# Performance work log

Hardware: AMD Instinct MI355X
Metric: run time of the kernel (lower is better)

## Reference

```python
import jax, jax.numpy as jnp
from jax import lax
import numpy as np

GROUPS = 32  # EMA 'factor'
EPS = 1e-5   # torch GroupNorm default eps


def setup_inputs() -> dict:
    key = jax.random.key(0)
    ks = jax.random.split(key, 3)
    B, C, H, W = 8, 256, 128, 128
    cg = C // GROUPS  # channels per group = 8
    x = jax.random.normal(ks[0], (B, C, H, W), dtype=jnp.float32)
    w1 = jax.random.normal(ks[1], (cg, cg), dtype=jnp.float32) * 0.1    # conv1x1 weight (O,I)
    b1 = jnp.zeros((cg,), dtype=jnp.float32)
    w3 = jax.random.normal(ks[2], (cg, cg, 3, 3), dtype=jnp.float32) * 0.1  # conv3x3 weight (O,I,kh,kw)
    b3 = jnp.zeros((cg,), dtype=jnp.float32)
    gn_w = jnp.ones((cg,), dtype=jnp.float32)
    gn_b = jnp.zeros((cg,), dtype=jnp.float32)
    return {"x": x, "w1": w1, "b1": b1, "w3": w3, "b3": b3, "gn_w": gn_w, "gn_b": gn_b}


def reference(x, w1, b1, w3, b3, gn_w, gn_b):
    b, c, h, w = x.shape
    g = GROUPS
    cg = c // g
    gx = x.reshape(b * g, cg, h, w)                       # [bg, cg, h, w]
    # directional pooling (AdaptiveAvgPool over one axis)
    x_h = gx.mean(axis=3, keepdims=True)                  # [bg, cg, h, 1]
    x_w = gx.mean(axis=2, keepdims=True).transpose(0, 1, 3, 2)  # [bg, cg, w, 1]
    hw = jnp.concatenate([x_h, x_w], axis=2)              # [bg, cg, h+w, 1]
    hw = jnp.einsum('oi,bilk->bolk', w1, hw) + b1[None, :, None, None]
    xh = hw[:, :, :h]                                      # [bg, cg, h, 1]
    xw = hw[:, :, h:].transpose(0, 1, 3, 2)                # [bg, cg, 1, w]
    gated = gx * jax.nn.sigmoid(xh) * jax.nn.sigmoid(xw)
    # GroupNorm(cg groups over cg channels) == per-channel norm over (h, w)
    mu = gated.mean(axis=(2, 3), keepdims=True)
    var = gated.var(axis=(2, 3), keepdims=True)
    x1 = (gated - mu) / jnp.sqrt(var + EPS) * gn_w[None, :, None, None] + gn_b[None, :, None, None]
    # 3x3 conv branch
    x2 = lax.conv_general_dilated(gx, w3, (1, 1), 'SAME',
                                  dimension_numbers=('NCHW', 'OIHW', 'NCHW'))
    x2 = x2 + b3[None, :, None, None]
    # cross-branch channel-attention matmuls
    x11 = jax.nn.softmax(x1.mean(axis=(2, 3)), axis=-1)[:, None, :]  # [bg, 1, cg]
    x21 = jax.nn.softmax(x2.mean(axis=(2, 3)), axis=-1)[:, None, :]  # [bg, 1, cg]
    x12 = x2.reshape(b * g, cg, h * w)
    x22 = x1.reshape(b * g, cg, h * w)
    weights = (jnp.matmul(x11, x12) + jnp.matmul(x21, x22)).reshape(b * g, 1, h, w)
    return (gx * jax.nn.sigmoid(weights)).reshape(b, c, h, w)
```

## Files before the change

kernel.cpp:

```cpp
#include <hip/hip_runtime.h>
#include <cstdint>

#define EPS 1e-5f

__global__ __launch_bounds__(256) void k1_sums(const float* __restrict__ x,
                                               float* __restrict__ rowsum,
                                               float* __restrict__ colsum) {
    int p = blockIdx.x;
    int t = threadIdx.x;
    const float4* xp = (const float4*)(x + (size_t)p * 16384);
    float4 csum = {0.f, 0.f, 0.f, 0.f};
    for (int i = 0; i < 16; ++i) {
        float4 v = xp[i * 256 + t];
        csum.x += v.x; csum.y += v.y; csum.z += v.z; csum.w += v.w;
        float rs = v.x + v.y + v.z + v.w;
        for (int m = 16; m; m >>= 1) rs += __shfl_xor(rs, m);
        if ((t & 31) == 0) rowsum[p * 128 + i * 8 + (t >> 5)] = rs;
    }
    __shared__ float4 red[256];
    red[t] = csum;
    __syncthreads();
    if (t < 32) {
        float4 s = red[t];
        for (int j = 1; j < 8; ++j) {
            float4 v = red[j * 32 + t];
            s.x += v.x; s.y += v.y; s.z += v.z; s.w += v.w;
        }
        ((float4*)colsum)[p * 32 + t] = s;
    }
}

__global__ __launch_bounds__(1024) void k2_mid(
    const float* __restrict__ x,
    const float* __restrict__ rowsum, const float* __restrict__ colsum,
    const float* __restrict__ w1, const float* __restrict__ b1,
    const float* __restrict__ w3, const float* __restrict__ b3,
    const float* __restrict__ gn_w, const float* __restrict__ gn_b,
    float* __restrict__ sh, float* __restrict__ sw,
    float* __restrict__ wt, float* __restrict__ alpha, float* __restrict__ beta)
{
    __shared__ float rs[1024], cs[1024], shl[1024], swl[1024];
    __shared__ float w1l[64], b1l[8], corn[32], S[8], Tm[72], m2[8], x11[8], x21l[8];
    __shared__ float ps[64], qs[64], bs[8];
    __shared__ float btl;
    const int bg = blockIdx.x;
    const int t  = threadIdx.x;
    const int sg = t >> 8, ts = t & 255;
    const size_t pbase = (size_t)(bg * 8) * 16384;

    rs[t] = rowsum[bg * 1024 + t];
    cs[t] = colsum[bg * 1024 + t];
    if (t < 64) w1l[t] = w1[t];
    if (t >= 64 && t < 72) b1l[t - 64] = b1[t - 64];
    if (t >= 128 && t < 136) {
        int i = t - 128;
        const float* xpp = x + pbase + (size_t)i * 16384;
        corn[i * 4 + 0] = xpp[0];
        corn[i * 4 + 1] = xpp[127];
        corn[i * 4 + 2] = xpp[127 * 128];
        corn[i * 4 + 3] = xpp[127 * 128 + 127];
    }
    if (t == 200) {
        float mx = gn_b[0];
        for (int i = 1; i < 8; ++i) mx = fmaxf(mx, gn_b[i]);
        float e[8], s = 0.f;
        for (int i = 0; i < 8; ++i) { e[i] = __expf(gn_b[i] - mx); s += e[i]; }
        for (int i = 0; i < 8; ++i) x11[i] = e[i] / s;
    }
    __syncthreads();

    if (t == 300) {
        float a = 0.f;
        for (int o = 0; o < 8; ++o) a += x11[o] * b3[o];
        btl = a;
    }
    {
        int o = t >> 7, y = t & 127;
        const float inv128 = 1.f / 128.f;
        float ar = b1l[o], ac = ar;
        for (int i = 0; i < 8; ++i) {
            float w = w1l[o * 8 + i];
            ar += w * rs[i * 128 + y] * inv128;
            ac += w * cs[i * 128 + y] * inv128;
        }
        float sv = 1.f / (1.f + __expf(-ar));
        float wv = 1.f / (1.f + __expf(-ac));
        shl[o * 128 + y] = sv;  sh[(bg * 8 + o) * 128 + y] = sv;
        swl[o * 128 + y] = wv;  sw[(bg * 8 + o) * 128 + y] = wv;
    }
    if (t < 8) {
        float s = 0.f;
        for (int y = 0; y < 128; ++y) s += rs[t * 128 + y];
        S[t] = s;
    }
    __syncthreads();

    if (t < 72) {
        int i = t / 9, ky = (t % 9) / 3, kx = t % 3;
        float v = S[i];
        if (ky == 0) v -= rs[i * 128 + 127]; else if (ky == 2) v -= rs[i * 128 + 0];
        if (kx == 0) v -= cs[i * 128 + 127]; else if (kx == 2) v -= cs[i * 128 + 0];
        if (ky == 0 && kx == 0) v += corn[i * 4 + 3];
        if (ky == 0 && kx == 2) v += corn[i * 4 + 2];
        if (ky == 2 && kx == 0) v += corn[i * 4 + 1];
        if (ky == 2 && kx == 2) v += corn[i * 4 + 0];
        Tm[t] = v;
    }
    __syncthreads();

    if (t < 8) {
        float acc = 0.f;
        for (int j = 0; j < 72; ++j) acc += w3[t * 72 + j] * Tm[j];
        m2[t] = b3[t] + acc * (1.f / 16384.f);
    }
    if (bg == 0 && t >= 128 && t < 200) {
        int j = t - 128;
        float a = 0.f;
        for (int o = 0; o < 8; ++o) a += x11[o] * w3[o * 72 + j];
        wt[j] = a;
    }
    __syncthreads();

    if (t == 0) {
        float mx = m2[0];
        for (int i = 1; i < 8; ++i) mx = fmaxf(mx, m2[i]);
        float e[8], s = 0.f;
        for (int i = 0; i < 8; ++i) { e[i] = __expf(m2[i] - mx); s += e[i]; }
        for (int i = 0; i < 8; ++i) x21l[i] = e[i] / s;
    }
    __syncthreads();

    for (int half = 0; half < 2; ++half) {
        int pi = half * 4 + sg;
        const float4* xp = (const float4*)(x + pbase + (size_t)pi * 16384);
        float4 sw4 = ((const float4*)(swl + pi * 128))[ts & 31];
        float s = 0.f, q = 0.f;
        for (int i = 0; i < 16; ++i) {
            float4 v = xp[i * 256 + ts];
            float shv = shl[pi * 128 + i * 8 + (ts >> 5)];
            float g0 = v.x * shv * sw4.x;
            float g1 = v.y * shv * sw4.y;
            float g2 = v.z * shv * sw4.z;
            float g3 = v.w * shv * sw4.w;
            s += g0 + g1 + g2 + g3;
            q += g0 * g0 + g1 * g1 + g2 * g2 + g3 * g3;
        }
        for (int m = 16; m; m >>= 1) { s += __shfl_xor(s, m); q += __shfl_xor(q, m); }
        if ((ts & 31) == 0) {
            ps[pi * 8 + (ts >> 5)] = s;
            qs[pi * 8 + (ts >> 5)] = q;
        }
    }
    __syncthreads();
    if (t < 8) {
        float s = 0.f, q = 0.f;
        for (int j = 0; j < 8; ++j) { s += ps[t * 8 + j]; q += qs[t * 8 + j]; }
        float mu  = s * (1.f / 16384.f);
        float ex2 = q * (1.f / 16384.f);
        float var = ex2 - mu * mu;
        float inv = rsqrtf(var + EPS);
        float x21v = x21l[t];
        alpha[bg * 8 + t] = x21v * inv * gn_w[t];
        bs[t] = x21v * (gn_b[t] - mu * inv * gn_w[t]);
    }
    __syncthreads();
    if (t == 0) {
        float s = btl;
        for (int i = 0; i < 8; ++i) s += bs[i];
        beta[bg] = s;
    }
}

__global__ __launch_bounds__(512, 4) void k3_out(
    const float* __restrict__ x, const float* __restrict__ sh,
    const float* __restrict__ sw, const float* __restrict__ alpha,
    const float* __restrict__ beta, const float* __restrict__ wt,
    float* __restrict__ out)
{
    __shared__ float tl[8 * 18 * 128];
    __shared__ float wtl[72], al[8], shl[128];
    __shared__ float betal;
    const int blk = blockIdx.x, bg = blk >> 3, r0 = (blk & 7) * 16;
    const int t = threadIdx.x, lane = t & 31, w = t >> 5;
    const size_t pbase = (size_t)(bg * 8) * 16384;

#pragma unroll
    for (int it = 0; it < 9; ++it) {
        int idx = it * 512 + t;
        int ch  = idx / 576;
        int rem = idx - ch * 576;
        int row = rem >> 5;
        int slot = rem & 31;
        int g = r0 - 1 + row;
        float4 v = {0.f, 0.f, 0.f, 0.f};
        if ((unsigned)g < 128u)
            v = *(const float4*)(x + pbase + (size_t)ch * 16384 + g * 128 + slot * 4);
        *(float4*)(tl + ch * 2304 + row * 128 + slot * 4) = v;
    }
    if (t < 72) wtl[t] = wt[t];
    if (t >= 128 && t < 136) al[t - 128] = alpha[bg * 8 + (t - 128)];
    if (t == 136) betal = beta[bg];
    if (t >= 256 && t < 384) {
        int u = t - 256;
        shl[u] = sh[(size_t)(bg * 8 + (u >> 4)) * 128 + r0 + (u & 15)];
    }
    __syncthreads();

    const int y  = r0 + w;
    const int x0 = lane * 4;
    float4 acc = {betal, betal, betal, betal};
    float4 gv[8];

#pragma unroll
    for (int ch = 0; ch < 8; ++ch) {
        const float* base = tl + ch * 2304 + w * 128 + x0;
#pragma unroll
        for (int r = 0; r < 3; ++r) {
            float4 va = *(const float4*)(base + r * 128);
            float xm1 = __shfl_up(va.w, 1, 32);   if (lane == 0)  xm1 = 0.f;
            float xp4 = __shfl_down(va.x, 1, 32); if (lane == 31) xp4 = 0.f;
            float w0 = wtl[ch * 9 + r * 3 + 0];
            float w1v = wtl[ch * 9 + r * 3 + 1];
            float w2 = wtl[ch * 9 + r * 3 + 2];
            acc.x += w0 * xm1  + w1v * va.x + w2 * va.y;
            acc.y += w0 * va.x + w1v * va.y + w2 * va.z;
            acc.z += w0 * va.y + w1v * va.z + w2 * va.w;
            acc.w += w0 * va.z + w1v * va.w + w2 * xp4;
            if (r == 1) gv[ch] = va;
        }
        float as = al[ch] * shl[(ch << 4) + w];
        float4 s4 = *(const float4*)(sw + (size_t)(bg * 8 + ch) * 128 + x0);
        acc.x += as * s4.x * gv[ch].x;
        acc.y += as * s4.y * gv[ch].y;
        acc.z += as * s4.z * gv[ch].z;
        acc.w += as * s4.w * gv[ch].w;
    }

    float4 sg;
    sg.x = 1.f / (1.f + __expf(-acc.x));
    sg.y = 1.f / (1.f + __expf(-acc.y));
    sg.z = 1.f / (1.f + __expf(-acc.z));
    sg.w = 1.f / (1.f + __expf(-acc.w));

    const size_t ob = pbase + (size_t)y * 128 + x0;
#pragma unroll
    for (int c = 0; c < 8; ++c) {
        float4 o4 = { gv[c].x * sg.x, gv[c].y * sg.y, gv[c].z * sg.z, gv[c].w * sg.w };
        *(float4*)(out + ob + (size_t)c * 16384) = o4;
    }
}

extern "C" void kernel_launch(void* const* d_in, const int* in_sizes, int n_in,
                              void* d_out, int out_size, void* d_ws, size_t ws_size,
                              hipStream_t stream) {
    (void)in_sizes; (void)n_in; (void)out_size; (void)ws_size;
    const float* x    = (const float*)d_in[0];
    const float* w1   = (const float*)d_in[1];
    const float* b1   = (const float*)d_in[2];
    const float* w3   = (const float*)d_in[3];
    const float* b3   = (const float*)d_in[4];
    const float* gn_w = (const float*)d_in[5];
    const float* gn_b = (const float*)d_in[6];
    float* out = (float*)d_out;
    float* ws  = (float*)d_ws;

    float* rowsum = ws;
    float* colsum = ws + 262144;
    float* sh     = ws + 524288;
    float* sw     = ws + 786432;
    float* alpha  = ws + 1048576;
    float* beta   = ws + 1050624;
    float* wt     = ws + 1050880;

    hipLaunchKernelGGL(k1_sums, dim3(2048), dim3(256),  0, stream, x, rowsum, colsum);
    hipLaunchKernelGGL(k2_mid,  dim3(256),  dim3(1024), 0, stream, x, rowsum, colsum,
                       w1, b1, w3, b3, gn_w, gn_b, sh, sw, wt, alpha, beta);
    hipLaunchKernelGGL(k3_out,  dim3(2048), dim3(512),  0, stream, x, sh, sw,
                       alpha, beta, wt, out);
}
```

Measured before the change: 103.9 us.

## Fuse row/column sum pass into the mid-stage kernel

```diff
diff --git a/kernel.cpp b/kernel.cpp
--- a/kernel.cpp
+++ b/kernel.cpp
@@ -3,36 +3,8 @@
 
 #define EPS 1e-5f
 
-__global__ __launch_bounds__(256) void k1_sums(const float* __restrict__ x,
-                                               float* __restrict__ rowsum,
-                                               float* __restrict__ colsum) {
-    int p = blockIdx.x;
-    int t = threadIdx.x;
-    const float4* xp = (const float4*)(x + (size_t)p * 16384);
-    float4 csum = {0.f, 0.f, 0.f, 0.f};
-    for (int i = 0; i < 16; ++i) {
-        float4 v = xp[i * 256 + t];
-        csum.x += v.x; csum.y += v.y; csum.z += v.z; csum.w += v.w;
-        float rs = v.x + v.y + v.z + v.w;
-        for (int m = 16; m; m >>= 1) rs += __shfl_xor(rs, m);
-        if ((t & 31) == 0) rowsum[p * 128 + i * 8 + (t >> 5)] = rs;
-    }
-    __shared__ float4 red[256];
-    red[t] = csum;
-    __syncthreads();
-    if (t < 32) {
-        float4 s = red[t];
-        for (int j = 1; j < 8; ++j) {
-            float4 v = red[j * 32 + t];
-            s.x += v.x; s.y += v.y; s.z += v.z; s.w += v.w;
-        }
-        ((float4*)colsum)[p * 32 + t] = s;
-    }
-}
-
-__global__ __launch_bounds__(1024) void k2_mid(
+__global__ __launch_bounds__(1024) void k1_mid(
     const float* __restrict__ x,
-    const float* __restrict__ rowsum, const float* __restrict__ colsum,
     const float* __restrict__ w1, const float* __restrict__ b1,
     const float* __restrict__ w3, const float* __restrict__ b3,
     const float* __restrict__ gn_w, const float* __restrict__ gn_b,
@@ -40,6 +12,7 @@
     float* __restrict__ wt, float* __restrict__ alpha, float* __restrict__ beta)
 {
     __shared__ float rs[1024], cs[1024], shl[1024], swl[1024];
+    __shared__ float4 red[1024];
     __shared__ float w1l[64], b1l[8], corn[32], S[8], Tm[72], m2[8], x11[8], x21l[8];
     __shared__ float ps[64], qs[64], bs[8];
     __shared__ float btl;
@@ -48,8 +21,30 @@
     const int sg = t >> 8, ts = t & 255;
     const size_t pbase = (size_t)(bg * 8) * 16384;
 
-    rs[t] = rowsum[bg * 1024 + t];
-    cs[t] = colsum[bg * 1024 + t];
+    for (int half = 0; half < 2; ++half) {
+        int pi = half * 4 + sg;
+        const float4* xp = (const float4*)(x + pbase + (size_t)pi * 16384);
+        float4 csum = {0.f, 0.f, 0.f, 0.f};
+        for (int i = 0; i < 16; ++i) {
+            float4 v = xp[i * 256 + ts];
+            csum.x += v.x; csum.y += v.y; csum.z += v.z; csum.w += v.w;
+            float rsv = v.x + v.y + v.z + v.w;
+            for (int m = 16; m; m >>= 1) rsv += __shfl_xor(rsv, m);
+            if ((ts & 31) == 0) rs[pi * 128 + i * 8 + (ts >> 5)] = rsv;
+        }
+        red[sg * 256 + ts] = csum;
+        __syncthreads();
+        if (ts < 32) {
+            float4 s = red[sg * 256 + ts];
+            for (int j = 1; j < 8; ++j) {
+                float4 v = red[sg * 256 + j * 32 + ts];
+                s.x += v.x; s.y += v.y; s.z += v.z; s.w += v.w;
+            }
+            ((float4*)(cs + pi * 128))[ts] = s;
+        }
+        __syncthreads();
+    }
+
     if (t < 64) w1l[t] = w1[t];
     if (t >= 64 && t < 72) b1l[t - 64] = b1[t - 64];
     if (t >= 128 && t < 136) {
@@ -171,7 +166,7 @@
     }
 }
 
-__global__ __launch_bounds__(512, 4) void k3_out(
+__global__ __launch_bounds__(512, 4) void k2_out(
     const float* __restrict__ x, const float* __restrict__ sh,
     const float* __restrict__ sw, const float* __restrict__ alpha,
     const float* __restrict__ beta, const float* __restrict__ wt,
@@ -264,17 +259,14 @@
     float* out = (float*)d_out;
     float* ws  = (float*)d_ws;
 
-    float* rowsum = ws;
-    float* colsum = ws + 262144;
-    float* sh     = ws + 524288;
-    float* sw     = ws + 786432;
-    float* alpha  = ws + 1048576;
-    float* beta   = ws + 1050624;
-    float* wt     = ws + 1050880;
-
-    hipLaunchKernelGGL(k1_sums, dim3(2048), dim3(256),  0, stream, x, rowsum, colsum);
-    hipLaunchKernelGGL(k2_mid,  dim3(256),  dim3(1024), 0, stream, x, rowsum, colsum,
+    float* sh    = ws;
+    float* sw    = ws + 262144;
+    float* alpha = ws + 524288;
+    float* beta  = ws + 526336;
+    float* wt    = ws + 526592;
+
+    hipLaunchKernelGGL(k1_mid, dim3(256),  dim3(1024), 0, stream, x,
                        w1, b1, w3, b3, gn_w, gn_b, sh, sw, wt, alpha, beta);
-    hipLaunchKernelGGL(k3_out,  dim3(2048), dim3(512),  0, stream, x, sh, sw,
+    hipLaunchKernelGGL(k2_out, dim3(2048), dim3(512),  0, stream, x, sh, sw,
                        alpha, beta, wt, out);
 }
```

After: 105.4 us. No clear change (+1.5%).
